# Kernel tuning notes

Hardware: AMD Instinct MI355X
Metric: run time of the kernel (lower is better)

## Reference

```python
import jax, jax.numpy as jnp
import numpy as np

NUM_HEADS = 16

def setup_inputs() -> dict:
    key = jax.random.key(0)
    ks = jax.random.split(key, 6)
    b, t, d = 2, 2048, 1024
    s = 0.02
    return {
        "x": jax.random.normal(ks[0], (b, t, d), jnp.float32),
        "Wq": jax.random.normal(ks[1], (d, d), jnp.float32) * s,
        "Wk": jax.random.normal(ks[2], (d, d), jnp.float32) * s,
        "Wv": jax.random.normal(ks[3], (d, d), jnp.float32) * s,
        "Wo": jax.random.normal(ks[4], (d, d), jnp.float32) * s,
        "bo": jnp.zeros((d,), jnp.float32),
    }

def reference(x, Wq, Wk, Wv, Wo, bo):
    b, t, d = x.shape
    h = NUM_HEADS
    hd = d // h  # head_dim = d_out / num_heads
    # torch nn.Linear: y = x @ W.T (qkv_bias=False)
    def split_heads(y):
        return y.reshape(b, t, h, hd).transpose(0, 2, 1, 3)  # [b,h,t,hd]
    q = split_heads(x @ Wq.T)
    k = split_heads(x @ Wk.T)
    v = split_heads(x @ Wv.T)
    scale = 1.0 / jnp.sqrt(jnp.asarray(hd, x.dtype))
    # NOTE: original forward computes but never applies the causal mask or dropout
    scores = jnp.einsum('bhqd,bhkd->bhqk', q, k) * scale
    attn = jax.nn.softmax(scores, axis=-1)
    ctx = jnp.einsum('bhqk,bhkd->bhqd', attn, v)
    ctx = ctx.transpose(0, 2, 1, 3).reshape(b, t, d)
    return ctx @ Wo.T + bo
```

## Files before the change

### kernel.cpp

```cpp
#include <hip/hip_runtime.h>
#include <hip/hip_bf16.h>
#include <math.h>
#include <stdint.h>
#include <string.h>

#define TSEQ 2048
#define DMODEL 1024
#define NH 16
#define HD 64
#define BROWS 4096
#define BH 32

typedef __attribute__((ext_vector_type(8))) short short8;
typedef __attribute__((ext_vector_type(4))) float floatx4;

#define MFMA16 __builtin_amdgcn_mfma_f32_16x16x32_bf16
#define SWZ8(r, q) ((((q) ^ ((r) & 7)) * 8))

#define QSCALE 0.18033688011112042f

__device__ __forceinline__ unsigned short bf16_rne(float f) {
    uint32_t u = __float_as_uint(f);
    u += 0x7FFFu + ((u >> 16) & 1u);
    return (unsigned short)(u >> 16);
}

__device__ __forceinline__ void split_bf16(float f, short& hi, short& lo) {
    uint32_t u = __float_as_uint(f);
    hi = (short)(u >> 16);
    float hif = __uint_as_float(u & 0xFFFF0000u);
    lo = (short)bf16_rne(f - hif);
}

__device__ __forceinline__ void async16(const void* g, void* l) {
    __builtin_amdgcn_global_load_lds(
        (__attribute__((address_space(1))) const uint32_t*)g,
        (__attribute__((address_space(3))) uint32_t*)l, 16, 0, 0);
}

struct PackArgs {
    const float4* x;
    ushort4* xb;
    const float4* w[3];
    ushort4* wb[3];
    const float4* wo;
    ushort4* woh;
    ushort4* wol;
};
__global__ __launch_bounds__(256) void pack_all(PackArgs a) {
    const int y = blockIdx.y;
    const int base = blockIdx.x * 256 + threadIdx.x;
    if (y == 0) {
#pragma unroll
        for (int it = 0; it < 4; ++it) {
            int i = base + it * 262144;
            float4 f = a.x[i];
            a.xb[i] = make_ushort4(bf16_rne(f.x), bf16_rne(f.y),
                                   bf16_rne(f.z), bf16_rne(f.w));
        }
    } else if (y <= 3) {
        int w = y - 1;
        float4 f = a.w[w][base];
        a.wb[w][base] = make_ushort4(bf16_rne(f.x), bf16_rne(f.y),
                                     bf16_rne(f.z), bf16_rne(f.w));
    } else {
        float4 f = a.wo[base];
        short h0, l0, h1, l1, h2, l2, h3, l3;
        split_bf16(f.x, h0, l0); split_bf16(f.y, h1, l1);
        split_bf16(f.z, h2, l2); split_bf16(f.w, h3, l3);
        a.woh[base] = make_ushort4(h0, h1, h2, h3);
        a.wol[base] = make_ushort4(l0, l1, l2, l3);
    }
}

__global__ __launch_bounds__(256) void gemm_qkv(
    const short* __restrict__ Xb,
    const short* __restrict__ Bq, const short* __restrict__ Bk,
    const short* __restrict__ Bv,
    short* __restrict__ Qo, short* __restrict__ Ko, short* __restrict__ Vo) {
    __shared__ short sA[128 * 64];
    __shared__ short sB[128 * 64];
    const int K = DMODEL;

    const int tid = threadIdx.x;
    const int lane = tid & 63, wave = tid >> 6;
    const int quad = lane >> 4, col = lane & 15;
    const int m0 = blockIdx.y * 128, n0 = blockIdx.x * 128;
    const int which = n0 >> 10;
    const int nn0 = n0 & 1023;
    const int wm = wave >> 1, wn = wave & 1;

    const short* B = (which == 0) ? Bq : (which == 1) ? Bk : Bv;
    const short* Asrc = Xb + (size_t)m0 * K;
    const short* Bsrc = B + (size_t)nn0 * K;

    const int srow = lane >> 3;
    const int soff = (((lane & 7) ^ srow) * 8);

    floatx4 acc[4][4] = {};

    for (int k0 = 0; k0 < K; k0 += 64) {
        __syncthreads();
#pragma unroll
        for (int j = 0; j < 8; ++j) {
            int idx = wave * 8 + j;
            int sub = idx & 15;
            const short* s = (idx < 16) ? Asrc : Bsrc;
            short* d = (idx < 16) ? sA : sB;
            async16(s + (size_t)(sub * 8 + srow) * K + k0 + soff, d + sub * 512);
        }
        __syncthreads();

#pragma unroll
        for (int s2 = 0; s2 < 2; ++s2) {
            short8 a_b[4], b_b[4];
#pragma unroll
            for (int mi = 0; mi < 4; ++mi) {
                int r = wm * 64 + mi * 16 + col;
                a_b[mi] = *(const short8*)&sA[r * 64 + SWZ8(r, s2 * 4 + quad)];
            }
#pragma unroll
            for (int ni = 0; ni < 4; ++ni) {
                int r = wn * 64 + ni * 16 + col;
                b_b[ni] = *(const short8*)&sB[r * 64 + SWZ8(r, s2 * 4 + quad)];
            }
#pragma unroll
            for (int mi = 0; mi < 4; ++mi)
#pragma unroll
                for (int ni = 0; ni < 4; ++ni)
                    acc[mi][ni] = MFMA16(a_b[mi], b_b[ni], acc[mi][ni], 0, 0, 0);
        }
    }

    const int mb = m0 + wm * 64;
    const int nlb = nn0 + wn * 64;
    if (which == 2) {
#pragma unroll
        for (int ni = 0; ni < 4; ++ni) {
            int n = nlb + ni * 16 + col;
            int h = n >> 6, hd = n & 63;
#pragma unroll
            for (int mi = 0; mi < 4; ++mi) {
                int m4 = mb + mi * 16 + quad * 4;
                int b = m4 >> 11, t0 = m4 & 2047;
                int chunk = (t0 >> 3) & 7;
                int tsw = (t0 & ~63) | (((chunk ^ (hd & 7)) << 3) | (t0 & 7));
                size_t row = ((size_t)(b * NH + h) * HD + hd) * TSEQ;
                *(ushort4*)&Vo[row + tsw] =
                    make_ushort4(bf16_rne(acc[mi][ni][0]), bf16_rne(acc[mi][ni][1]),
                                 bf16_rne(acc[mi][ni][2]), bf16_rne(acc[mi][ni][3]));
            }
        }
    } else {
        short* O = (which == 0) ? Qo : Ko;
        const float sc = (which == 0) ? QSCALE : 1.0f;
#pragma unroll
        for (int ni = 0; ni < 4; ++ni) {
            int n = nlb + ni * 16 + col;
            int h = n >> 6, hd = n & 63;
#pragma unroll
            for (int mi = 0; mi < 4; ++mi)
#pragma unroll
                for (int r = 0; r < 4; ++r) {
                    int m = mb + mi * 16 + quad * 4 + r;
                    int b = m >> 11, t = m & 2047;
                    int hds = (which == 1) ? ((((hd >> 3) ^ (t & 7)) << 3) | (hd & 7)) : hd;
                    O[((size_t)(b * NH + h) * TSEQ + t) * HD + hds] =
                        bf16_rne(acc[mi][ni][r] * sc);
                }
        }
    }
}

__global__ __launch_bounds__(512) void attn_bf16(
    const short* __restrict__ Qb, const short* __restrict__ Kb,
    const short* __restrict__ Vb, short* __restrict__ Cb) {
    __shared__ short sK[2][64 * 64];
    __shared__ short sV[2][64 * 64];
    __shared__ short sP[8][16 * 72];

    const int tid = threadIdx.x;
    const int lane = tid & 63, wave = tid >> 6;
    const int quad = lane >> 4, col = lane & 15;
    const int qt = blockIdx.x, bh = blockIdx.y;
    const size_t bhoff = (size_t)bh * TSEQ * HD;

    const size_t qrow = (size_t)(qt * 128 + wave * 16 + col) * HD;
    short8 qf[2];
#pragma unroll
    for (int c = 0; c < 2; ++c)
        qf[c] = *(const short8*)&Qb[bhoff + qrow + c * 32 + quad * 8];

    const int srow = lane >> 3;
    const int schunk = (lane & 7) * 8;

    float l_r[4] = {};
    floatx4 O[4] = {};

    for (int kt = 0; kt < 16; ++kt) {
        __syncthreads();
#pragma unroll
        for (int j = 0; j < 4; ++j) {
            int n = wave * 4 + j;
            int isv = n >> 4;
            int tile = (n >> 3) & 1;
            int sub = n & 7;
            if (!isv) {
                async16(Kb + bhoff + (size_t)(kt * 128 + tile * 64 + sub * 8 + srow) * HD + schunk,
                        &sK[tile][sub * 512]);
            } else {
                async16(Vb + bhoff + (size_t)(sub * 8 + srow) * TSEQ + kt * 128 + tile * 64 + schunk,
                        &sV[tile][sub * 512]);
            }
        }
        __syncthreads();

#pragma unroll
        for (int u = 0; u < 2; ++u) {
            floatx4 s[4] = {};
#pragma unroll
            for (int ni = 0; ni < 4; ++ni) {
                int r = ni * 16 + col;
#pragma unroll
                for (int c = 0; c < 2; ++c) {
                    int ch = (((c * 4 + quad) ^ (r & 7)) << 3);
                    short8 kf = *(const short8*)&sK[u][r * 64 + ch];
                    s[ni] = MFMA16(qf[c], kf, s[ni], 0, 0, 0);
                }
            }

#pragma unroll
            for (int ni = 0; ni < 4; ++ni)
#pragma unroll
                for (int r = 0; r < 4; ++r) {
                    float p = __builtin_amdgcn_exp2f(s[ni][r]);
                    l_r[r] += p;
                    sP[wave][(quad * 4 + r) * 72 + ni * 16 + col] = (short)bf16_rne(p);
                }

#pragma unroll
            for (int c = 0; c < 2; ++c) {
                short8 pf = *(const short8*)&sP[wave][col * 72 + c * 32 + quad * 8];
#pragma unroll
                for (int ni = 0; ni < 4; ++ni) {
                    int r = ni * 16 + col;
                    int ch = (((c * 4 + quad) ^ (r & 7)) << 3);
                    short8 vf = *(const short8*)&sV[u][r * 64 + ch];
                    O[ni] = MFMA16(pf, vf, O[ni], 0, 0, 0);
                }
            }
        }
    }

#pragma unroll
    for (int r = 0; r < 4; ++r) {
        float t = l_r[r];
#pragma unroll
        for (int d = 1; d < 16; d <<= 1) t += __shfl_xor(t, d);
        l_r[r] = 1.0f / t;
    }
    const int b = bh >> 4, h = bh & 15;
#pragma unroll
    for (int r = 0; r < 4; ++r) {
        int t = qt * 128 + wave * 16 + quad * 4 + r;
#pragma unroll
        for (int ni = 0; ni < 4; ++ni) {
            int d = h * 64 + ni * 16 + col;
            Cb[(size_t)(b * TSEQ + t) * DMODEL + d] = bf16_rne(O[ni][r] * l_r[r]);
        }
    }
}

__global__ __launch_bounds__(256) void gemm_out(
    const short* __restrict__ Ab,
    const short* __restrict__ Bh, const short* __restrict__ Bl,
    const float* __restrict__ bias, float* __restrict__ Of) {
    __shared__ short sA[128 * 64];
    __shared__ short sBh[64 * 64];
    __shared__ short sBl[64 * 64];
    const int K = DMODEL, N = DMODEL;

    const int tid = threadIdx.x;
    const int lane = tid & 63, wave = tid >> 6;
    const int quad = lane >> 4, col = lane & 15;
    const int m0 = blockIdx.y * 128, n0 = blockIdx.x * 64;
    const int wm = wave >> 1, wn = wave & 1;

    const short* Asrc = Ab + (size_t)m0 * K;
    const short* Bhsrc = Bh + (size_t)n0 * K;
    const short* Blsrc = Bl + (size_t)n0 * K;
    const int srow = lane >> 3;
    const int soff = (((lane & 7) ^ srow) * 8);

    floatx4 acc[4][2] = {};

    for (int k0 = 0; k0 < K; k0 += 64) {
        __syncthreads();
#pragma unroll
        for (int j = 0; j < 8; ++j) {
            int idx = wave * 8 + j;
            int buf = (idx < 16) ? 0 : (idx < 24) ? 1 : 2;
            int sub = (buf == 0) ? idx : (buf == 1) ? idx - 16 : idx - 24;
            const short* s = (buf == 0) ? Asrc : (buf == 1) ? Bhsrc : Blsrc;
            short* d = (buf == 0) ? sA : (buf == 1) ? sBh : sBl;
            async16(s + (size_t)(sub * 8 + srow) * K + k0 + soff, d + sub * 512);
        }
        __syncthreads();

#pragma unroll
        for (int s2 = 0; s2 < 2; ++s2) {
            short8 a_b[4], b_h[2], b_l[2];
#pragma unroll
            for (int mi = 0; mi < 4; ++mi) {
                int r = wm * 64 + mi * 16 + col;
                a_b[mi] = *(const short8*)&sA[r * 64 + SWZ8(r, s2 * 4 + quad)];
            }
#pragma unroll
            for (int ni = 0; ni < 2; ++ni) {
                int r = wn * 32 + ni * 16 + col;
                b_h[ni] = *(const short8*)&sBh[r * 64 + SWZ8(r, s2 * 4 + quad)];
                b_l[ni] = *(const short8*)&sBl[r * 64 + SWZ8(r, s2 * 4 + quad)];
            }
#pragma unroll
            for (int mi = 0; mi < 4; ++mi)
#pragma unroll
                for (int ni = 0; ni < 2; ++ni) {
                    acc[mi][ni] = MFMA16(a_b[mi], b_h[ni], acc[mi][ni], 0, 0, 0);
                    acc[mi][ni] = MFMA16(a_b[mi], b_l[ni], acc[mi][ni], 0, 0, 0);
                }
        }
    }

    const int mb = m0 + wm * 64, nb = n0 + wn * 32;
#pragma unroll
    for (int ni = 0; ni < 2; ++ni) {
        int n = nb + ni * 16 + col;
        float bv = bias[n];
#pragma unroll
        for (int mi = 0; mi < 4; ++mi)
#pragma unroll
            for (int r = 0; r < 4; ++r) {
                int m = mb + mi * 16 + quad * 4 + r;
                Of[(size_t)m * N + n] = acc[mi][ni][r] + bv;
            }
    }
}

extern "C" void kernel_launch(void* const* d_in, const int* in_sizes, int n_in,
                              void* d_out, int out_size, void* d_ws, size_t ws_size,
                              hipStream_t stream) {
    const float* x  = (const float*)d_in[0];
    const float* Wq = (const float*)d_in[1];
    const float* Wk = (const float*)d_in[2];
    const float* Wv = (const float*)d_in[3];
    const float* Wo = (const float*)d_in[4];
    const float* bo = (const float*)d_in[5];
    float* out = (float*)d_out;

    const size_t NX = (size_t)BROWS * DMODEL;
    const size_t NW = (size_t)DMODEL * DMODEL;
    short* p = (short*)d_ws;
    short *xb = p;
    short *wqb = xb + NX;
    short *wkb = wqb + NW;
    short *wvb = wkb + NW;
    short *woh = wvb + NW; short *wol = woh + NW;
    short *qb = wol + NW;
    short *kb = qb + NX;
    short *vb = kb + NX;
    short *cb = vb + NX;

    PackArgs pa;
    pa.x = (const float4*)x; pa.xb = (ushort4*)xb;
    pa.w[0] = (const float4*)Wq; pa.wb[0] = (ushort4*)wqb;
    pa.w[1] = (const float4*)Wk; pa.wb[1] = (ushort4*)wkb;
    pa.w[2] = (const float4*)Wv; pa.wb[2] = (ushort4*)wvb;
    pa.wo = (const float4*)Wo; pa.woh = (ushort4*)woh; pa.wol = (ushort4*)wol;
    pack_all<<<dim3(1024, 5), dim3(256), 0, stream>>>(pa);

    gemm_qkv<<<dim3(3 * DMODEL / 128, BROWS / 128), dim3(256), 0, stream>>>(
        xb, wqb, wkb, wvb, qb, kb, vb);

    attn_bf16<<<dim3(TSEQ / 128, BH), dim3(512), 0, stream>>>(qb, kb, vb, cb);

    gemm_out<<<dim3(DMODEL / 64, BROWS / 128), dim3(256), 0, stream>>>(cb, woh, wol, bo, out);
}
```

Measured before the change: 209.6 us.

## Transpose MFMA operands so accumulators hold contiguous columns for vector stores

Swaps the A/B operands of the MFMA calls in the Q/K projection, attention and output GEMM kernels, so each lane's four accumulator values lie along the feature dimension rather than along rows. This lets epilogues write packed ushort4/uint2/float4 stores instead of scalar ones. In attention, the softmax row sum becomes a single per-lane value reduced with two shuffles, and the P tile moves to an unpadded XOR-swizzled LDS layout written with packed bf16x2 stores. The intent is fewer store instructions and fewer LDS transactions, at the cost of more complex swizzle indexing.

```diff
diff --git a/kernel.cpp b/kernel.cpp
--- a/kernel.cpp
+++ b/kernel.cpp
@@ -23,6 +23,13 @@
     uint32_t u = __float_as_uint(f);
     u += 0x7FFFu + ((u >> 16) & 1u);
     return (unsigned short)(u >> 16);
+}
+
+__device__ __forceinline__ uint32_t pack_bf16x2(float a, float b) {
+    __hip_bfloat162 h = __float22bfloat162_rn(float2{a, b});
+    uint32_t r;
+    memcpy(&r, &h, 4);
+    return r;
 }
 
 __device__ __forceinline__ void split_bf16(float f, short& hi, short& lo) {
@@ -124,11 +131,19 @@
                 int r = wn * 64 + ni * 16 + col;
                 b_b[ni] = *(const short8*)&sB[r * 64 + SWZ8(r, s2 * 4 + quad)];
             }
-#pragma unroll
-            for (int mi = 0; mi < 4; ++mi)
-#pragma unroll
-                for (int ni = 0; ni < 4; ++ni)
-                    acc[mi][ni] = MFMA16(a_b[mi], b_b[ni], acc[mi][ni], 0, 0, 0);
+            if (which == 2) {
+#pragma unroll
+                for (int mi = 0; mi < 4; ++mi)
+#pragma unroll
+                    for (int ni = 0; ni < 4; ++ni)
+                        acc[mi][ni] = MFMA16(a_b[mi], b_b[ni], acc[mi][ni], 0, 0, 0);
+            } else {
+#pragma unroll
+                for (int mi = 0; mi < 4; ++mi)
+#pragma unroll
+                    for (int ni = 0; ni < 4; ++ni)
+                        acc[mi][ni] = MFMA16(b_b[ni], a_b[mi], acc[mi][ni], 0, 0, 0);
+            }
         }
     }
 
@@ -155,19 +170,19 @@
         short* O = (which == 0) ? Qo : Ko;
         const float sc = (which == 0) ? QSCALE : 1.0f;
 #pragma unroll
-        for (int ni = 0; ni < 4; ++ni) {
-            int n = nlb + ni * 16 + col;
-            int h = n >> 6, hd = n & 63;
-#pragma unroll
-            for (int mi = 0; mi < 4; ++mi)
-#pragma unroll
-                for (int r = 0; r < 4; ++r) {
-                    int m = mb + mi * 16 + quad * 4 + r;
-                    int b = m >> 11, t = m & 2047;
-                    int hds = (which == 1) ? ((((hd >> 3) ^ (t & 7)) << 3) | (hd & 7)) : hd;
-                    O[((size_t)(b * NH + h) * TSEQ + t) * HD + hds] =
-                        bf16_rne(acc[mi][ni][r] * sc);
-                }
+        for (int mi = 0; mi < 4; ++mi) {
+            int m = mb + mi * 16 + col;
+            int b = m >> 11, t = m & 2047;
+#pragma unroll
+            for (int ni = 0; ni < 4; ++ni) {
+                int n = nlb + ni * 16 + quad * 4;
+                int h = n >> 6, hd = n & 63;
+                int hds = (which == 1) ? ((((hd >> 3) ^ (t & 7)) << 3) | (hd & 7)) : hd;
+                size_t idx = ((size_t)(b * NH + h) * TSEQ + t) * HD + hds;
+                *(ushort4*)&O[idx] =
+                    make_ushort4(bf16_rne(acc[mi][ni][0] * sc), bf16_rne(acc[mi][ni][1] * sc),
+                                 bf16_rne(acc[mi][ni][2] * sc), bf16_rne(acc[mi][ni][3] * sc));
+            }
         }
     }
 }
@@ -177,7 +192,7 @@
     const short* __restrict__ Vb, short* __restrict__ Cb) {
     __shared__ short sK[2][64 * 64];
     __shared__ short sV[2][64 * 64];
-    __shared__ short sP[8][16 * 72];
+    __shared__ short sP[8][16 * 64];
 
     const int tid = threadIdx.x;
     const int lane = tid & 63, wave = tid >> 6;
@@ -193,8 +208,9 @@
 
     const int srow = lane >> 3;
     const int schunk = (lane & 7) * 8;
-
-    float l_r[4] = {};
+    short* sPw = sP[wave];
+
+    float l_r = 0.f;
     floatx4 O[4] = {};
 
     for (int kt = 0; kt < 16; ++kt) {
@@ -219,55 +235,59 @@
         for (int u = 0; u < 2; ++u) {
             floatx4 s[4] = {};
 #pragma unroll
-            for (int ni = 0; ni < 4; ++ni) {
-                int r = ni * 16 + col;
+            for (int k4 = 0; k4 < 4; ++k4) {
+                int r = k4 * 16 + col;
 #pragma unroll
                 for (int c = 0; c < 2; ++c) {
                     int ch = (((c * 4 + quad) ^ (r & 7)) << 3);
                     short8 kf = *(const short8*)&sK[u][r * 64 + ch];
-                    s[ni] = MFMA16(qf[c], kf, s[ni], 0, 0, 0);
+                    s[k4] = MFMA16(kf, qf[c], s[k4], 0, 0, 0);
                 }
             }
 
 #pragma unroll
-            for (int ni = 0; ni < 4; ++ni)
-#pragma unroll
-                for (int r = 0; r < 4; ++r) {
-                    float p = __builtin_amdgcn_exp2f(s[ni][r]);
-                    l_r[r] += p;
-                    sP[wave][(quad * 4 + r) * 72 + ni * 16 + col] = (short)bf16_rne(p);
-                }
+            for (int k4 = 0; k4 < 4; ++k4) {
+                float p0 = __builtin_amdgcn_exp2f(s[k4][0]);
+                float p1 = __builtin_amdgcn_exp2f(s[k4][1]);
+                float p2 = __builtin_amdgcn_exp2f(s[k4][2]);
+                float p3 = __builtin_amdgcn_exp2f(s[k4][3]);
+                l_r += (p0 + p1) + (p2 + p3);
+                uint2 pk;
+                pk.x = pack_bf16x2(p0, p1);
+                pk.y = pack_bf16x2(p2, p3);
+                int swz = (k4 * 2 + (quad >> 1)) ^ (col & 7);
+                *(uint2*)&sPw[col * 64 + swz * 8 + (quad & 1) * 4] = pk;
+            }
 
 #pragma unroll
             for (int c = 0; c < 2; ++c) {
-                short8 pf = *(const short8*)&sP[wave][col * 72 + c * 32 + quad * 8];
+                int pswz = ((c * 4 + quad) ^ (col & 7)) * 8;
+                short8 pf = *(const short8*)&sPw[col * 64 + pswz];
 #pragma unroll
                 for (int ni = 0; ni < 4; ++ni) {
                     int r = ni * 16 + col;
                     int ch = (((c * 4 + quad) ^ (r & 7)) << 3);
                     short8 vf = *(const short8*)&sV[u][r * 64 + ch];
-                    O[ni] = MFMA16(pf, vf, O[ni], 0, 0, 0);
+                    O[ni] = MFMA16(vf, pf, O[ni], 0, 0, 0);
                 }
             }
         }
     }
 
-#pragma unroll
-    for (int r = 0; r < 4; ++r) {
-        float t = l_r[r];
-#pragma unroll
-        for (int d = 1; d < 16; d <<= 1) t += __shfl_xor(t, d);
-        l_r[r] = 1.0f / t;
-    }
+    float t = l_r;
+    t += __shfl_xor(t, 16);
+    t += __shfl_xor(t, 32);
+    const float inv = 1.0f / t;
+
     const int b = bh >> 4, h = bh & 15;
-#pragma unroll
-    for (int r = 0; r < 4; ++r) {
-        int t = qt * 128 + wave * 16 + quad * 4 + r;
-#pragma unroll
-        for (int ni = 0; ni < 4; ++ni) {
-            int d = h * 64 + ni * 16 + col;
-            Cb[(size_t)(b * TSEQ + t) * DMODEL + d] = bf16_rne(O[ni][r] * l_r[r]);
-        }
+    const int trow = qt * 128 + wave * 16 + col;
+    const size_t obase = (size_t)(b * TSEQ + trow) * DMODEL + h * 64;
+#pragma unroll
+    for (int ni = 0; ni < 4; ++ni) {
+        uint2 pk;
+        pk.x = pack_bf16x2(O[ni][0] * inv, O[ni][1] * inv);
+        pk.y = pack_bf16x2(O[ni][2] * inv, O[ni][3] * inv);
+        *(uint2*)&Cb[obase + ni * 16 + quad * 4] = pk;
     }
 }
 
@@ -325,24 +345,24 @@
             for (int mi = 0; mi < 4; ++mi)
 #pragma unroll
                 for (int ni = 0; ni < 2; ++ni) {
-                    acc[mi][ni] = MFMA16(a_b[mi], b_h[ni], acc[mi][ni], 0, 0, 0);
-                    acc[mi][ni] = MFMA16(a_b[mi], b_l[ni], acc[mi][ni], 0, 0, 0);
+                    acc[mi][ni] = MFMA16(b_h[ni], a_b[mi], acc[mi][ni], 0, 0, 0);
+                    acc[mi][ni] = MFMA16(b_l[ni], a_b[mi], acc[mi][ni], 0, 0, 0);
                 }
         }
     }
 
     const int mb = m0 + wm * 64, nb = n0 + wn * 32;
 #pragma unroll
-    for (int ni = 0; ni < 2; ++ni) {
-        int n = nb + ni * 16 + col;
-        float bv = bias[n];
-#pragma unroll
-        for (int mi = 0; mi < 4; ++mi)
-#pragma unroll
-            for (int r = 0; r < 4; ++r) {
-                int m = mb + mi * 16 + quad * 4 + r;
-                Of[(size_t)m * N + n] = acc[mi][ni][r] + bv;
-            }
+    for (int mi = 0; mi < 4; ++mi) {
+        int m = mb + mi * 16 + col;
+#pragma unroll
+        for (int ni = 0; ni < 2; ++ni) {
+            int n = nb + ni * 16 + quad * 4;
+            float4 bv = *(const float4*)&bias[n];
+            float4 o = make_float4(acc[mi][ni][0] + bv.x, acc[mi][ni][1] + bv.y,
+                                   acc[mi][ni][2] + bv.z, acc[mi][ni][3] + bv.w);
+            *(float4*)&Of[(size_t)m * N + n] = o;
+        }
     }
 }
 
```

New measurement: 199.6 us. 1.05x faster.
